# Kernel optimization log

Measured on AMD Instinct MI355X. Metric: run time of the kernel, lower is better.

The kernel has to match this reference:

```python
import jax, jax.numpy as jnp
import numpy as np

T, B, IN, H = 2048, 2048, 5, 10


def setup_inputs() -> dict:
    key = jax.random.key(0)
    ks = jax.random.split(key, 7)
    return {
        "x": jax.random.normal(ks[0], (T, B, IN), dtype=jnp.float32),
        "hx0": jax.random.uniform(ks[1], (B, H), dtype=jnp.float32),
        "cx0": jax.random.uniform(ks[2], (B, H), dtype=jnp.float32),
        "W_ih": jax.random.normal(ks[3], (4 * H, IN), dtype=jnp.float32) * 0.3,
        "W_hh": jax.random.normal(ks[4], (4 * H, H), dtype=jnp.float32) * 0.3,
        "b_ih": jax.random.normal(ks[5], (4 * H,), dtype=jnp.float32) * 0.1,
        "b_hh": jax.random.normal(ks[6], (4 * H,), dtype=jnp.float32) * 0.1,
    }


def reference(x, hx0, cx0, W_ih, W_hh, b_ih, b_hh):
    # torch.nn.LSTMCell gate order: i, f, g, o
    bias = b_ih + b_hh  # [4H]

    def step(carry, xt):
        h, c = carry  # [B, H] each
        gates = xt @ W_ih.T + h @ W_hh.T + bias  # [B, 4H]
        i, f, g, o = jnp.split(gates, 4, axis=-1)
        c_new = jax.nn.sigmoid(f) * c + jax.nn.sigmoid(i) * jnp.tanh(g)
        h_new = jax.nn.sigmoid(o) * jnp.tanh(c_new)
        return (h_new, c_new), h_new

    _, hs = jax.lax.scan(step, (hx0, cx0), x)  # hs: [T, B, H]
    # original concatenates per-step hx along dim 0 -> [T*B, H]
    return hs.reshape(-1, hs.shape[-1])
```

## Files before the change

### kernel.cpp

```cpp
#include <hip/hip_runtime.h>


#define T_STEPS 2048
#define BATCH   2048
#define NIN     5
#define NH      10
#define PF      4

typedef float v2f __attribute__((ext_vector_type(2)));

__device__ __forceinline__ float hw_exp2(float v) { return __builtin_amdgcn_exp2f(v); }
__device__ __forceinline__ float hw_rcp(float v)  { return __builtin_amdgcn_rcpf(v); }
__device__ __forceinline__ float readlane_f(float v, int srclane) {
    return __builtin_bit_cast(float,
        __builtin_amdgcn_readlane(__builtin_bit_cast(int, v), srclane));
}
__device__ __forceinline__ v2f splat2(float v) { v2f r; r.x = v; r.y = v; return r; }

__global__ __launch_bounds__(64, 1) void lstm_fused_kernel(
    const float* __restrict__ x,   const float* __restrict__ hx0,
    const float* __restrict__ cx0, const float* __restrict__ Wih,
    const float* __restrict__ Whh, const float* __restrict__ bih,
    const float* __restrict__ bhh, float* __restrict__ out)
{
    const float L2E2  = 2.8853900817779268f;
    const float NL2E  = -1.4426950408889634f;
    const float NL2E2 = -2.8853900817779268f;

    const int lane = threadIdx.x;
    const int half = lane >> 5;
    int j = lane & 31;
    if (j > NH - 1) j = NH - 1;
    const bool lo = (lane < 32);

    const int b = blockIdx.x * 2 + half;

    const int ri = j, rf = NH + j, rg = 2 * NH + j, ro = 3 * NH + j;

    v2f wxif[NIN], wxgo[NIN], whif[NH], whgo[NH];
#pragma unroll
    for (int k = 0; k < NIN; ++k) {
        wxif[k].x = NL2E  * Wih[ri * NIN + k];  wxif[k].y = NL2E * Wih[rf * NIN + k];
        wxgo[k].x = NL2E2 * Wih[rg * NIN + k];  wxgo[k].y = NL2E * Wih[ro * NIN + k];
    }
#pragma unroll
    for (int k = 0; k < NH; ++k) {
        whif[k].x = NL2E  * Whh[ri * NH + k];   whif[k].y = NL2E * Whh[rf * NH + k];
        whgo[k].x = NL2E2 * Whh[rg * NH + k];   whgo[k].y = NL2E * Whh[ro * NH + k];
    }
    v2f bif, bgo;
    bif.x = NL2E  * (bih[ri] + bhh[ri]);  bif.y = NL2E * (bih[rf] + bhh[rf]);
    bgo.x = NL2E2 * (bih[rg] + bhh[rg]);  bgo.y = NL2E * (bih[ro] + bhh[ro]);

    float hv[NH];
#pragma unroll
    for (int k = 0; k < NH; ++k) hv[k] = hx0[b * NH + k];
    float cs2 = NL2E2 * cx0[b * NH + j];

    const float* xb = x + (size_t)b * NIN;
    float xr[PF][NIN];
#pragma unroll
    for (int q = 0; q < PF; ++q)
#pragma unroll
        for (int k = 0; k < NIN; ++k)
            xr[q][k] = xb[q * (BATCH * NIN) + k];

    float* outp = out + (size_t)b * NH + j;

#define LSTM_STEP(QQ, TT, DO_REFILL)                                          \
    {                                                                         \
                                                \
        v2f aif0 = bif, ago0 = bgo;                                           \
        v2f aif1 = splat2(0.0f), ago1 = splat2(0.0f);                         \
        {                                                                     \
            v2f xx0 = splat2(xr[QQ][0]);                                      \
            v2f xx1 = splat2(xr[QQ][1]);                                      \
            v2f xx2 = splat2(xr[QQ][2]);                                      \
            v2f xx3 = splat2(xr[QQ][3]);                                      \
            v2f xx4 = splat2(xr[QQ][4]);                                      \
            aif0 += xx0 * wxif[0];  ago0 += xx0 * wxgo[0];                    \
            aif1 += xx1 * wxif[1];  ago1 += xx1 * wxgo[1];                    \
            aif0 += xx2 * wxif[2];  ago0 += xx2 * wxgo[2];                    \
            aif1 += xx3 * wxif[3];  ago1 += xx3 * wxgo[3];                    \
            aif0 += xx4 * wxif[4];  ago0 += xx4 * wxgo[4];                    \
        }                                                                     \
        if (DO_REFILL) {                                                      \
            const int tn = (TT) + PF;       \
            _Pragma("unroll")                                                 \
            for (int k = 0; k < NIN; ++k)                                     \
                xr[QQ][k] = xb[tn * (BATCH * NIN) + k];                       \
        }                                                                     \
             \
        _Pragma("unroll")                                                     \
        for (int k = 0; k < NH; k += 2) {                                     \
            v2f h0 = splat2(hv[k]);                                           \
            v2f h1 = splat2(hv[k + 1]);                                       \
            aif0 += h0 * whif[k];      ago0 += h0 * whgo[k];                  \
            aif1 += h1 * whif[k + 1];  ago1 += h1 * whgo[k + 1];              \
        }                                                                     \
        const v2f aif = aif0 + aif1;                                          \
        const v2f ago = ago0 + ago1;                                          \
                          \
        const float si  = hw_rcp(1.0f + hw_exp2(aif.x));                      \
        const float sf  = hw_rcp(1.0f + hw_exp2(aif.y));                      \
        const float rg_ = hw_rcp(1.0f + hw_exp2(ago.x));                      \
        const float so  = hw_rcp(1.0f + hw_exp2(ago.y));                      \
        const float tg2 = fmaf(-2.0f * L2E2, rg_, L2E2);   \
        cs2 = fmaf(sf, cs2, si * tg2);            \
        const float tc = fmaf(2.0f, hw_rcp(1.0f + hw_exp2(cs2)), -1.0f);      \
        const float h  = so * tc;                                             \
             \
        outp[(TT) * (BATCH * NH)] = h;                                        \
                 \
        _Pragma("unroll")                                                     \
        for (int k = 0; k < NH; ++k) {                                        \
            const float hA = readlane_f(h, k);                                \
            const float hB = readlane_f(h, 32 + k);                           \
            hv[k] = lo ? hA : hB;                                             \
        }                                                                     \
    }

#pragma unroll 1
    for (int t0 = 0; t0 < T_STEPS - PF; t0 += PF) {
        LSTM_STEP(0, t0 + 0, 1)
        LSTM_STEP(1, t0 + 1, 1)
        LSTM_STEP(2, t0 + 2, 1)
        LSTM_STEP(3, t0 + 3, 1)
    }
    {
        const int t0 = T_STEPS - PF;
        LSTM_STEP(0, t0 + 0, 0)
        LSTM_STEP(1, t0 + 1, 0)
        LSTM_STEP(2, t0 + 2, 0)
        LSTM_STEP(3, t0 + 3, 0)
    }
#undef LSTM_STEP
}

extern "C" void kernel_launch(void* const* d_in, const int* in_sizes, int n_in,
                              void* d_out, int out_size, void* d_ws, size_t ws_size,
                              hipStream_t stream) {
    const float* x   = (const float*)d_in[0];
    const float* hx0 = (const float*)d_in[1];
    const float* cx0 = (const float*)d_in[2];
    const float* Wih = (const float*)d_in[3];
    const float* Whh = (const float*)d_in[4];
    const float* bih = (const float*)d_in[5];
    const float* bhh = (const float*)d_in[6];
    float* out = (float*)d_out;

    lstm_fused_kernel<<<BATCH / 2, 64, 0, stream>>>(x, hx0, cx0, Wih, Whh, bih, bhh, out);
}
```

Before: 858.4 us.

## Split LSTM gates across lane groups, one batch row per wavefront

Each wavefront now handles one batch element instead of two. Its four 16-lane groups each compute one gate (i, f, g, o) with scalar FMAs, and ds_bpermute gathers the gate activations back to the lanes that update the cell state. This shortens the per-step dependency chain, since each lane does a quarter of the dot-product and activation work. The cost is twice as many wavefronts, four LDS permutes per step, and dropping the occupancy hint in launch_bounds.

Result: faster. 753.1 us (-12.3%).

```diff
diff --git a/kernel.cpp b/kernel.cpp
--- a/kernel.cpp
+++ b/kernel.cpp
@@ -7,17 +7,18 @@
 #define NH      10
 #define PF      4
 
-typedef float v2f __attribute__((ext_vector_type(2)));
-
 __device__ __forceinline__ float hw_exp2(float v) { return __builtin_amdgcn_exp2f(v); }
 __device__ __forceinline__ float hw_rcp(float v)  { return __builtin_amdgcn_rcpf(v); }
 __device__ __forceinline__ float readlane_f(float v, int srclane) {
     return __builtin_bit_cast(float,
         __builtin_amdgcn_readlane(__builtin_bit_cast(int, v), srclane));
 }
-__device__ __forceinline__ v2f splat2(float v) { v2f r; r.x = v; r.y = v; return r; }
+__device__ __forceinline__ float bperm_f(int byteidx, float v) {
+    return __builtin_bit_cast(float,
+        __builtin_amdgcn_ds_bpermute(byteidx, __builtin_bit_cast(int, v)));
+}
 
-__global__ __launch_bounds__(64, 1) void lstm_fused_kernel(
+__global__ __launch_bounds__(64) void lstm_fused_kernel(
     const float* __restrict__ x,   const float* __restrict__ hx0,
     const float* __restrict__ cx0, const float* __restrict__ Wih,
     const float* __restrict__ Whh, const float* __restrict__ bih,
@@ -28,29 +29,29 @@
     const float NL2E2 = -2.8853900817779268f;
 
     const int lane = threadIdx.x;
-    const int half = lane >> 5;
-    int j = lane & 31;
+    const int g    = lane >> 4;
+    int j = lane & 15;
     if (j > NH - 1) j = NH - 1;
-    const bool lo = (lane < 32);
 
-    const int b = blockIdx.x * 2 + half;
+    const int b = blockIdx.x;
 
-    const int ri = j, rf = NH + j, rg = 2 * NH + j, ro = 3 * NH + j;
+    const int r = g * NH + j;
+    const float scale = (g == 2) ? NL2E2 : NL2E;
 
-    v2f wxif[NIN], wxgo[NIN], whif[NH], whgo[NH];
+    float wx[NIN], wh[NH];
 #pragma unroll
-    for (int k = 0; k < NIN; ++k) {
-        wxif[k].x = NL2E  * Wih[ri * NIN + k];  wxif[k].y = NL2E * Wih[rf * NIN + k];
-        wxgo[k].x = NL2E2 * Wih[rg * NIN + k];  wxgo[k].y = NL2E * Wih[ro * NIN + k];
-    }
+    for (int k = 0; k < NIN; ++k) wx[k] = scale * Wih[r * NIN + k];
 #pragma unroll
-    for (int k = 0; k < NH; ++k) {
-        whif[k].x = NL2E  * Whh[ri * NH + k];   whif[k].y = NL2E * Whh[rf * NH + k];
-        whgo[k].x = NL2E2 * Whh[rg * NH + k];   whgo[k].y = NL2E * Whh[ro * NH + k];
-    }
-    v2f bif, bgo;
-    bif.x = NL2E  * (bih[ri] + bhh[ri]);  bif.y = NL2E * (bih[rf] + bhh[rf]);
-    bgo.x = NL2E2 * (bih[rg] + bhh[rg]);  bgo.y = NL2E * (bih[ro] + bhh[ro]);
+    for (int k = 0; k < NH; ++k)  wh[k] = scale * Whh[r * NH + k];
+    const float bb = scale * (bih[r] + bhh[r]);
+
+    const float cA = (g == 2) ? (-2.0f * L2E2) : 1.0f;
+    const float cB = (g == 2) ? L2E2 : 0.0f;
+
+    const int idx_i = j * 4;
+    const int idx_f = (16 + j) * 4;
+    const int idx_g = (32 + j) * 4;
+    const int idx_o = (48 + j) * 4;
 
     float hv[NH];
 #pragma unroll
@@ -69,55 +70,42 @@
 
 #define LSTM_STEP(QQ, TT, DO_REFILL)                                          \
     {                                                                         \
-                                                \
-        v2f aif0 = bif, ago0 = bgo;                                           \
-        v2f aif1 = splat2(0.0f), ago1 = splat2(0.0f);                         \
-        {                                                                     \
-            v2f xx0 = splat2(xr[QQ][0]);                                      \
-            v2f xx1 = splat2(xr[QQ][1]);                                      \
-            v2f xx2 = splat2(xr[QQ][2]);                                      \
-            v2f xx3 = splat2(xr[QQ][3]);                                      \
-            v2f xx4 = splat2(xr[QQ][4]);                                      \
-            aif0 += xx0 * wxif[0];  ago0 += xx0 * wxgo[0];                    \
-            aif1 += xx1 * wxif[1];  ago1 += xx1 * wxgo[1];                    \
-            aif0 += xx2 * wxif[2];  ago0 += xx2 * wxgo[2];                    \
-            aif1 += xx3 * wxif[3];  ago1 += xx3 * wxgo[3];                    \
-            aif0 += xx4 * wxif[4];  ago0 += xx4 * wxgo[4];                    \
-        }                                                                     \
+        \
+        float a0 = fmaf(wx[0], xr[QQ][0], bb);                                \
+        float a1 = wx[1] * xr[QQ][1];                                         \
+        a0 = fmaf(wx[2], xr[QQ][2], a0);                                      \
+        a1 = fmaf(wx[3], xr[QQ][3], a1);                                      \
+        a0 = fmaf(wx[4], xr[QQ][4], a0);                                      \
         if (DO_REFILL) {                                                      \
-            const int tn = (TT) + PF;       \
+            const int tn = (TT) + PF;                                         \
             _Pragma("unroll")                                                 \
             for (int k = 0; k < NIN; ++k)                                     \
                 xr[QQ][k] = xb[tn * (BATCH * NIN) + k];                       \
         }                                                                     \
-             \
         _Pragma("unroll")                                                     \
         for (int k = 0; k < NH; k += 2) {                                     \
-            v2f h0 = splat2(hv[k]);                                           \
-            v2f h1 = splat2(hv[k + 1]);                                       \
-            aif0 += h0 * whif[k];      ago0 += h0 * whgo[k];                  \
-            aif1 += h1 * whif[k + 1];  ago1 += h1 * whgo[k + 1];              \
+            a0 = fmaf(wh[k],     hv[k],     a0);                              \
+            a1 = fmaf(wh[k + 1], hv[k + 1], a1);                              \
         }                                                                     \
-        const v2f aif = aif0 + aif1;                                          \
-        const v2f ago = ago0 + ago1;                                          \
-                          \
-        const float si  = hw_rcp(1.0f + hw_exp2(aif.x));                      \
-        const float sf  = hw_rcp(1.0f + hw_exp2(aif.y));                      \
-        const float rg_ = hw_rcp(1.0f + hw_exp2(ago.x));                      \
-        const float so  = hw_rcp(1.0f + hw_exp2(ago.y));                      \
-        const float tg2 = fmaf(-2.0f * L2E2, rg_, L2E2);   \
-        cs2 = fmaf(sf, cs2, si * tg2);            \
+        const float a = a0 + a1;                                              \
+           \
+        const float s = hw_rcp(1.0f + hw_exp2(a));                            \
+        const float v = fmaf(cA, s, cB);                                      \
+                      \
+        const float vi = bperm_f(idx_i, v);                                   \
+        const float vf = bperm_f(idx_f, v);                                   \
+        const float vg = bperm_f(idx_g, v);                                   \
+        const float vo = bperm_f(idx_o, v);                                   \
+           \
+        cs2 = fmaf(vf, cs2, vi * vg);                                         \
         const float tc = fmaf(2.0f, hw_rcp(1.0f + hw_exp2(cs2)), -1.0f);      \
-        const float h  = so * tc;                                             \
-             \
+        const float h  = vo * tc;                                             \
+                \
         outp[(TT) * (BATCH * NH)] = h;                                        \
                  \
         _Pragma("unroll")                                                     \
-        for (int k = 0; k < NH; ++k) {                                        \
-            const float hA = readlane_f(h, k);                                \
-            const float hB = readlane_f(h, 32 + k);                           \
-            hv[k] = lo ? hA : hB;                                             \
-        }                                                                     \
+        for (int k = 0; k < NH; ++k)                                          \
+            hv[k] = readlane_f(h, k);                                         \
     }
 
 #pragma unroll 1
@@ -149,5 +137,5 @@
     const float* bhh = (const float*)d_in[6];
     float* out = (float*)d_out;
 
-    lstm_fused_kernel<<<BATCH / 2, 64, 0, stream>>>(x, hx0, cx0, Wih, Whh, bih, bhh, out);
+    lstm_fused_kernel<<<BATCH, 64, 0, stream>>>(x, hx0, cx0, Wih, Whh, bih, bhh, out);
 }
```
